# Kernel optimization log

Hardware: AMD Instinct MI355X
Metric: run time of the kernel (lower is better)

The kernel has to match this reference:

```python
import jax, jax.numpy as jnp
import numpy as np

N = 100000
E = 1600000
C = 128
NEG_SLOPE = 0.2
BN_EPS = 1e-5


def setup_inputs() -> dict:
    key = jax.random.key(0)
    ks = jax.random.split(key, 6)
    x = jax.random.normal(ks[0], (N, C), dtype=jnp.float32)
    edge_index = jax.random.randint(ks[1], (2, E), 0, N, dtype=jnp.int64)
    # Glorot-ish scaled params, stacked over the 3 layers (all 128->128)
    Ws = jax.random.normal(ks[2], (3, C, C), dtype=jnp.float32) * (1.0 / np.sqrt(C))
    att_srcs = jax.random.normal(ks[3], (3, C), dtype=jnp.float32) * (1.0 / np.sqrt(C))
    att_dsts = jax.random.normal(ks[4], (3, C), dtype=jnp.float32) * (1.0 / np.sqrt(C))
    biases = jnp.zeros((3, C), dtype=jnp.float32)
    gammas = jnp.ones((3, C), dtype=jnp.float32)
    betas = jnp.zeros((3, C), dtype=jnp.float32)
    return {"x": x, "edge_index": edge_index, "Ws": Ws, "att_srcs": att_srcs,
            "att_dsts": att_dsts, "biases": biases, "gammas": gammas, "betas": betas}


def _gat_layer(x, W, a_src, a_dst, bias, src, dst):
    # linear transform: [N, C]
    h = x @ W
    # per-node attention logits
    s_src = h @ a_src  # [N]
    s_dst = h @ a_dst  # [N]
    # edge-wise gather + leaky relu scoring
    e = jax.nn.leaky_relu(s_src[src] + s_dst[dst], NEG_SLOPE)  # [E+N]
    # scatter-softmax over incoming edges of each target node
    m = jax.ops.segment_max(e, dst, num_segments=N)  # every node has a self-loop
    ex = jnp.exp(e - m[dst])
    denom = jax.ops.segment_sum(ex, dst, num_segments=N)
    alpha = ex / denom[dst]  # [E+N]
    # scatter-add aggregation of alpha-weighted source features
    out = jax.ops.segment_sum(alpha[:, None] * h[src], dst, num_segments=N)
    return out + bias


def _batch_norm(x, gamma, beta):
    mu = jnp.mean(x, axis=0)
    var = jnp.mean(jnp.square(x - mu), axis=0)
    return gamma * (x - mu) * jax.lax.rsqrt(var + BN_EPS) + beta


def reference(x, edge_index, Ws, att_srcs, att_dsts, biases, gammas, betas):
    # PyG GATConv adds self-loops by default
    loops = jnp.arange(N, dtype=edge_index.dtype)
    src = jnp.concatenate([edge_index[0], loops])
    dst = jnp.concatenate([edge_index[1], loops])
    outs = []
    for l in range(3):
        x = _gat_layer(x, Ws[l], att_srcs[l], att_dsts[l], biases[l], src, dst)
        x = jax.nn.relu(x)
        x = _batch_norm(x, gammas[l], betas[l])
        outs.append(x)
    # jump=True: concat all layer outputs -> [N, 3*C]
    return jnp.concatenate(outs, axis=-1)
```

## Files before the change

kernel.cpp:

```cpp
#include <hip/hip_runtime.h>
#include <math.h>

#define N_NODES 100000
#define N_EDGES 1600000
#define M_TOT   (N_EDGES + N_NODES)
#define C_DIM   128
#define NEG_SLOPE 0.2f
#define BN_EPS 1e-5f

#define NBUCK 8
#define BUCK_NODES 12500
#define BUCK_CAP 240000

#define BN_NB 256
#define SCAN_NB 98

typedef _Float16 f16x8 __attribute__((ext_vector_type(8)));
typedef float f32x4 __attribute__((ext_vector_type(4)));

static __device__ __forceinline__ unsigned short f2h(float f) {
    _Float16 h = (_Float16)f;
    unsigned short u;
    __builtin_memcpy(&u, &h, 2);
    return u;
}
static __device__ __forceinline__ float h2f(unsigned short u) {
    _Float16 h;
    __builtin_memcpy(&h, &u, 2);
    return (float)h;
}
static __device__ __forceinline__ _Float16 f2h16(float f) { return (_Float16)f; }

__global__ void zero_i32(int* __restrict__ p, int n) {
    int i = blockIdx.x * blockDim.x + threadIdx.x;
    if (i < n) p[i] = 0;
}

__global__ __launch_bounds__(256) void conv_w(const float* __restrict__ Wall,
                                              unsigned short* __restrict__ Wh) {
    int i = blockIdx.x * 256 + threadIdx.x;
    if (i >= 3 * 128 * 128) return;
    int l = i >> 14;
    int r = i & 16383;
    int k = r >> 7;
    int n = r & 127;
    Wh[(size_t)l * 16384 + n * 128 + k] = f2h(Wall[i]);
}

__global__ __launch_bounds__(256) void bucket_edges(const int* __restrict__ ei,
                                                    int* __restrict__ bucket_next,
                                                    int2* __restrict__ buckets) {
    __shared__ int cnt[NBUCK];
    __shared__ int base[NBUCK];
    int tid = threadIdx.x;
    if (tid < NBUCK) cnt[tid] = 0;
    __syncthreads();
    int m = blockIdx.x * 256 + tid;
    int src = 0, dst = 0, p = 0, myoff = 0;
    bool valid = (m < M_TOT);
    if (valid) {
        if (m < N_EDGES) { src = ei[m]; dst = ei[N_EDGES + m]; }
        else             { src = m - N_EDGES; dst = src; }
        p = dst / BUCK_NODES;
        myoff = atomicAdd(&cnt[p], 1);
    }
    __syncthreads();
    if (tid < NBUCK) base[tid] = (cnt[tid] > 0) ? atomicAdd(&bucket_next[tid], cnt[tid]) : 0;
    __syncthreads();
    if (valid) {
        buckets[(size_t)p * BUCK_CAP + base[p] + myoff] = make_int2(src, dst);
    }
}

__global__ __launch_bounds__(256) void count_deg_b(const int2* __restrict__ buckets,
                                                   const int* __restrict__ bucket_next,
                                                   int* __restrict__ deg) {
    int p = blockIdx.x & 7;
    int chunk = blockIdx.x >> 3;
    int len = bucket_next[p];
    const int2* b = buckets + (size_t)p * BUCK_CAP;
    int stride = (gridDim.x >> 3) * 256;
    for (int i = chunk * 256 + threadIdx.x; i < len; i += stride) {
        atomicAdd(&deg[b[i].y], 1);
    }
}

__global__ __launch_bounds__(256) void scatter_b(const int2* __restrict__ buckets,
                                                 const int* __restrict__ bucket_next,
                                                 int* __restrict__ nextp,
                                                 int* __restrict__ csr_src) {
    int p = blockIdx.x & 7;
    int chunk = blockIdx.x >> 3;
    int len = bucket_next[p];
    const int2* b = buckets + (size_t)p * BUCK_CAP;
    int stride = (gridDim.x >> 3) * 256;
    for (int i = chunk * 256 + threadIdx.x; i < len; i += stride) {
        int2 e = b[i];
        int pos = atomicAdd(&nextp[e.y], 1);
        csr_src[pos] = e.x;
    }
}

__global__ __launch_bounds__(256) void block_sums(const int* __restrict__ deg,
                                                  int* __restrict__ partials) {
    __shared__ int lds[256];
    int base = blockIdx.x * 1024;
    int s = 0;
    for (int i = threadIdx.x; i < 1024; i += 256) {
        int idx = base + i;
        if (idx < N_NODES) s += deg[idx];
    }
    lds[threadIdx.x] = s;
    __syncthreads();
    for (int off = 128; off > 0; off >>= 1) {
        if (threadIdx.x < off) lds[threadIdx.x] += lds[threadIdx.x + off];
        __syncthreads();
    }
    if (threadIdx.x == 0) partials[blockIdx.x] = lds[0];
}

__global__ __launch_bounds__(128) void scan_partials(int* __restrict__ partials, int nb,
                                                     int* __restrict__ row_ptr) {
    __shared__ int lds[128];
    int tid = threadIdx.x;
    int v = (tid < nb) ? partials[tid] : 0;
    lds[tid] = v;
    __syncthreads();
    for (int off = 1; off < 128; off <<= 1) {
        int t = (tid >= off) ? lds[tid - off] : 0;
        __syncthreads();
        lds[tid] += t;
        __syncthreads();
    }
    if (tid < nb) partials[tid] = lds[tid] - v;
    if (tid == 0) row_ptr[N_NODES] = M_TOT;
}

__global__ __launch_bounds__(256) void scan_write(const int* __restrict__ deg,
                                                  const int* __restrict__ partials,
                                                  int* __restrict__ row_ptr,
                                                  int* __restrict__ nextp) {
    __shared__ int lds[256];
    int tid = threadIdx.x;
    int base = blockIdx.x * 1024;
    int i0 = base + tid * 4;
    int d[4];
#pragma unroll
    for (int t = 0; t < 4; ++t)
        d[t] = (i0 + t < N_NODES) ? deg[i0 + t] : 0;
    int tsum = d[0] + d[1] + d[2] + d[3];
    lds[tid] = tsum;
    __syncthreads();
    for (int off = 1; off < 256; off <<= 1) {
        int v = (tid >= off) ? lds[tid - off] : 0;
        __syncthreads();
        lds[tid] += v;
        __syncthreads();
    }
    int excl = lds[tid] - tsum;
    int run = partials[blockIdx.x] + excl;
#pragma unroll
    for (int t = 0; t < 4; ++t) {
        if (i0 + t < N_NODES) {
            row_ptr[i0 + t] = run;
            nextp[i0 + t]   = run;
            run += d[t];
        }
    }
}

__global__ __launch_bounds__(256, 2) void gemm_attn(
    const float* __restrict__ X, int ldx,
    const unsigned short* __restrict__ Wh,
    const float* __restrict__ a_src, const float* __restrict__ a_dst,
    const float* __restrict__ gbv,
    float* __restrict__ outw,
    unsigned short* __restrict__ Hh, float* __restrict__ Ssrc,
    float* __restrict__ Sdst) {
    int tid = threadIdx.x;
    int wave = tid >> 6;
    int lane = tid & 63;
    int q = lane >> 4;
    int l15 = lane & 15;
    int wrow = wave * 32;
    int rbase = blockIdx.x * 128;

    int row0 = rbase + wrow + l15;
    int row1 = row0 + 16;
    bool ok0 = row0 < N_NODES, ok1 = row1 < N_NODES;
    int r0c = ok0 ? row0 : (N_NODES - 1);
    int r1c = ok1 ? row1 : (N_NODES - 1);

    f32x4 acc[2][8] = {};

#pragma unroll
    for (int ks = 0; ks < 128; ks += 32) {
        int k0 = ks + q * 8;
        float4 v0 = *(const float4*)&X[(size_t)r0c * ldx + k0];
        float4 v1 = *(const float4*)&X[(size_t)r0c * ldx + k0 + 4];
        float4 u0 = *(const float4*)&X[(size_t)r1c * ldx + k0];
        float4 u1 = *(const float4*)&X[(size_t)r1c * ldx + k0 + 4];
        if (gbv) {
            float4 g0 = *(const float4*)&gbv[k0];
            float4 g1 = *(const float4*)&gbv[k0 + 4];
            float4 b0 = *(const float4*)&gbv[128 + k0];
            float4 b1 = *(const float4*)&gbv[128 + k0 + 4];
            v0.x = fmaf(v0.x, g0.x, b0.x); v0.y = fmaf(v0.y, g0.y, b0.y);
            v0.z = fmaf(v0.z, g0.z, b0.z); v0.w = fmaf(v0.w, g0.w, b0.w);
            v1.x = fmaf(v1.x, g1.x, b1.x); v1.y = fmaf(v1.y, g1.y, b1.y);
            v1.z = fmaf(v1.z, g1.z, b1.z); v1.w = fmaf(v1.w, g1.w, b1.w);
            u0.x = fmaf(u0.x, g0.x, b0.x); u0.y = fmaf(u0.y, g0.y, b0.y);
            u0.z = fmaf(u0.z, g0.z, b0.z); u0.w = fmaf(u0.w, g0.w, b0.w);
            u1.x = fmaf(u1.x, g1.x, b1.x); u1.y = fmaf(u1.y, g1.y, b1.y);
            u1.z = fmaf(u1.z, g1.z, b1.z); u1.w = fmaf(u1.w, g1.w, b1.w);
            if (ok0) {
                *(float4*)&outw[(size_t)row0 * 384 + k0] = v0;
                *(float4*)&outw[(size_t)row0 * 384 + k0 + 4] = v1;
            }
            if (ok1) {
                *(float4*)&outw[(size_t)row1 * 384 + k0] = u0;
                *(float4*)&outw[(size_t)row1 * 384 + k0 + 4] = u1;
            }
        }
        f16x8 a0, a1;
        a0[0] = f2h16(v0.x); a0[1] = f2h16(v0.y); a0[2] = f2h16(v0.z); a0[3] = f2h16(v0.w);
        a0[4] = f2h16(v1.x); a0[5] = f2h16(v1.y); a0[6] = f2h16(v1.z); a0[7] = f2h16(v1.w);
        a1[0] = f2h16(u0.x); a1[1] = f2h16(u0.y); a1[2] = f2h16(u0.z); a1[3] = f2h16(u0.w);
        a1[4] = f2h16(u1.x); a1[5] = f2h16(u1.y); a1[6] = f2h16(u1.z); a1[7] = f2h16(u1.w);
#pragma unroll
        for (int c = 0; c < 8; ++c) {
            f16x8 b = *(const f16x8*)&Wh[(size_t)(c * 16 + l15) * 128 + k0];
            acc[0][c] = __builtin_amdgcn_mfma_f32_16x16x32_f16(a0, b, acc[0][c], 0, 0, 0);
            acc[1][c] = __builtin_amdgcn_mfma_f32_16x16x32_f16(a1, b, acc[1][c], 0, 0, 0);
        }
    }

    float avs[8], avd[8];
#pragma unroll
    for (int c = 0; c < 8; ++c) {
        avs[c] = a_src[c * 16 + l15];
        avd[c] = a_dst[c * 16 + l15];
    }
#pragma unroll
    for (int r = 0; r < 2; ++r) {
        float ps[4] = {0, 0, 0, 0}, pd[4] = {0, 0, 0, 0};
#pragma unroll
        for (int g = 0; g < 4; ++g) {
            int row = rbase + wrow + r * 16 + q * 4 + g;
            bool ok = (row < N_NODES);
#pragma unroll
            for (int c = 0; c < 8; ++c) {
                float h = acc[r][c][g];
                if (ok) Hh[(size_t)row * 128 + c * 16 + l15] = f2h(h);
                ps[g] = fmaf(h, avs[c], ps[g]);
                pd[g] = fmaf(h, avd[c], pd[g]);
            }
        }
#pragma unroll
        for (int g = 0; g < 4; ++g) {
#pragma unroll
            for (int off = 1; off < 16; off <<= 1) {
                ps[g] += __shfl_xor(ps[g], off, 64);
                pd[g] += __shfl_xor(pd[g], off, 64);
            }
        }
        if (l15 == 0) {
#pragma unroll
            for (int g = 0; g < 4; ++g) {
                int row = rbase + wrow + r * 16 + q * 4 + g;
                if (row < N_NODES) {
                    Ssrc[row] = ps[g];
                    Sdst[row] = pd[g];
                }
            }
        }
    }
}

__global__ __launch_bounds__(256) void aggregate(
    const unsigned short* __restrict__ Hh, const int* __restrict__ row_ptr,
    const int* __restrict__ csr_src,
    const float* __restrict__ Ssrc, const float* __restrict__ Sdst,
    const float* __restrict__ bias, float* __restrict__ Y) {
    int wave = threadIdx.x >> 6;
    int lane = threadIdx.x & 63;
    int g = lane >> 4;
    int l15 = lane & 15;
    int v = blockIdx.x * 4 + wave;
    int start = row_ptr[v];
    int end = row_ptr[v + 1];
    float sdv = Sdst[v];

    float sself = Ssrc[v] + sdv;
    float m = (sself > 0.0f) ? sself : NEG_SLOPE * sself;

    float acc[8] = {0, 0, 0, 0, 0, 0, 0, 0};
    float denom = 0.0f;

    int j = start;
    for (; j + 16 <= end; j += 16) {
        int u0 = csr_src[j + g];
        int u1 = csr_src[j + 4 + g];
        int u2 = csr_src[j + 8 + g];
        int u3 = csr_src[j + 12 + g];
        float ss0 = Ssrc[u0];
        float ss1 = Ssrc[u1];
        float ss2 = Ssrc[u2];
        float ss3 = Ssrc[u3];
        f16x8 h0 = *(const f16x8*)&Hh[(size_t)u0 * 128 + l15 * 8];
        f16x8 h1 = *(const f16x8*)&Hh[(size_t)u1 * 128 + l15 * 8];
        f16x8 h2 = *(const f16x8*)&Hh[(size_t)u2 * 128 + l15 * 8];
        f16x8 h3 = *(const f16x8*)&Hh[(size_t)u3 * 128 + l15 * 8];
        float s0 = ss0 + sdv; s0 = (s0 > 0.0f) ? s0 : NEG_SLOPE * s0;
        float s1 = ss1 + sdv; s1 = (s1 > 0.0f) ? s1 : NEG_SLOPE * s1;
        float s2 = ss2 + sdv; s2 = (s2 > 0.0f) ? s2 : NEG_SLOPE * s2;
        float s3 = ss3 + sdv; s3 = (s3 > 0.0f) ? s3 : NEG_SLOPE * s3;
        float w0 = __expf(s0 - m);
        float w1 = __expf(s1 - m);
        float w2 = __expf(s2 - m);
        float w3 = __expf(s3 - m);
        denom += (w0 + w1) + (w2 + w3);
#pragma unroll
        for (int i = 0; i < 8; ++i) acc[i] = fmaf(w0, (float)h0[i], acc[i]);
#pragma unroll
        for (int i = 0; i < 8; ++i) acc[i] = fmaf(w1, (float)h1[i], acc[i]);
#pragma unroll
        for (int i = 0; i < 8; ++i) acc[i] = fmaf(w2, (float)h2[i], acc[i]);
#pragma unroll
        for (int i = 0; i < 8; ++i) acc[i] = fmaf(w3, (float)h3[i], acc[i]);
    }
    for (; j + 8 <= end; j += 8) {
        int u0 = csr_src[j + g];
        int u1 = csr_src[j + 4 + g];
        float ss0 = Ssrc[u0];
        float ss1 = Ssrc[u1];
        f16x8 h0 = *(const f16x8*)&Hh[(size_t)u0 * 128 + l15 * 8];
        f16x8 h1 = *(const f16x8*)&Hh[(size_t)u1 * 128 + l15 * 8];
        float s0 = ss0 + sdv; s0 = (s0 > 0.0f) ? s0 : NEG_SLOPE * s0;
        float s1 = ss1 + sdv; s1 = (s1 > 0.0f) ? s1 : NEG_SLOPE * s1;
        float w0 = __expf(s0 - m);
        float w1 = __expf(s1 - m);
        denom += w0 + w1;
#pragma unroll
        for (int i = 0; i < 8; ++i) acc[i] = fmaf(w0, (float)h0[i], acc[i]);
#pragma unroll
        for (int i = 0; i < 8; ++i) acc[i] = fmaf(w1, (float)h1[i], acc[i]);
    }
    for (; j < end; j += 4) {
        int je = j + g;
        bool ok = (je < end);
        int u = ok ? csr_src[je] : v;
        float s = Ssrc[u] + sdv; s = (s > 0.0f) ? s : NEG_SLOPE * s;
        float w = ok ? __expf(s - m) : 0.0f;
        f16x8 h = *(const f16x8*)&Hh[(size_t)u * 128 + l15 * 8];
        denom += w;
#pragma unroll
        for (int i = 0; i < 8; ++i) acc[i] = fmaf(w, (float)h[i], acc[i]);
    }

#pragma unroll
    for (int i = 0; i < 8; ++i) {
        acc[i] += __shfl_xor(acc[i], 16, 64);
        acc[i] += __shfl_xor(acc[i], 32, 64);
    }
    denom += __shfl_xor(denom, 16, 64);
    denom += __shfl_xor(denom, 32, 64);

    if (g == 0) {
        float inv = 1.0f / denom;
        float4 b0 = *(const float4*)&bias[l15 * 8];
        float4 b1 = *(const float4*)&bias[l15 * 8 + 4];
        float4 o0, o1;
        o0.x = fmaxf(fmaf(acc[0], inv, b0.x), 0.0f);
        o0.y = fmaxf(fmaf(acc[1], inv, b0.y), 0.0f);
        o0.z = fmaxf(fmaf(acc[2], inv, b0.z), 0.0f);
        o0.w = fmaxf(fmaf(acc[3], inv, b0.w), 0.0f);
        o1.x = fmaxf(fmaf(acc[4], inv, b1.x), 0.0f);
        o1.y = fmaxf(fmaf(acc[5], inv, b1.y), 0.0f);
        o1.z = fmaxf(fmaf(acc[6], inv, b1.z), 0.0f);
        o1.w = fmaxf(fmaf(acc[7], inv, b1.w), 0.0f);
        *(float4*)&Y[(size_t)v * 128 + l15 * 8] = o0;
        *(float4*)&Y[(size_t)v * 128 + l15 * 8 + 4] = o1;
    }
}

__global__ __launch_bounds__(256) void bn_stats(const float* __restrict__ Y,
                                                float* __restrict__ partial) {
    __shared__ float red[256 * 8];
    int tid = threadIdx.x;
    int rowlane = tid >> 5;
    int cg = tid & 31;
    float4 s = make_float4(0, 0, 0, 0);
    float4 qq = make_float4(0, 0, 0, 0);
    for (int i = blockIdx.x * 8 + rowlane; i < N_NODES; i += BN_NB * 8) {
        float4 v = *(const float4*)&Y[(size_t)i * 128 + cg * 4];
        s.x += v.x; s.y += v.y; s.z += v.z; s.w += v.w;
        qq.x = fmaf(v.x, v.x, qq.x);
        qq.y = fmaf(v.y, v.y, qq.y);
        qq.z = fmaf(v.z, v.z, qq.z);
        qq.w = fmaf(v.w, v.w, qq.w);
    }
    float* r = &red[tid * 8];
    r[0] = s.x; r[1] = s.y; r[2] = s.z; r[3] = s.w;
    r[4] = qq.x; r[5] = qq.y; r[6] = qq.z; r[7] = qq.w;
    __syncthreads();
    for (int off = 4; off > 0; off >>= 1) {
        if (rowlane < off) {
            float* o = &red[(tid + off * 32) * 8];
#pragma unroll
            for (int t = 0; t < 8; ++t) r[t] += o[t];
        }
        __syncthreads();
    }
    if (rowlane == 0) {
        *(float4*)&partial[(size_t)blockIdx.x * 256 + cg * 4] =
            make_float4(r[0], r[1], r[2], r[3]);
        *(float4*)&partial[(size_t)blockIdx.x * 256 + 128 + cg * 4] =
            make_float4(r[4], r[5], r[6], r[7]);
    }
}

__global__ __launch_bounds__(256) void bn_finalize(const float* __restrict__ partial,
                                                   const float* __restrict__ gamma,
                                                   const float* __restrict__ beta,
                                                   float* __restrict__ gb) {
    __shared__ float tot[256];
    int tid = threadIdx.x;
    float acc = 0.0f;
    for (int b = 0; b < BN_NB; ++b) acc += partial[(size_t)b * 256 + tid];
    tot[tid] = acc;
    __syncthreads();
    if (tid < 128) {
        const float invN = 1.0f / (float)N_NODES;
        float mu = tot[tid] * invN;
        float var = tot[128 + tid] * invN - mu * mu;
        float g = gamma[tid] * rsqrtf(var + BN_EPS);
        gb[tid] = g;
        gb[128 + tid] = beta[tid] - mu * g;
    }
}

__global__ __launch_bounds__(256) void bn_apply(const float* __restrict__ Y,
                                                const float* __restrict__ gb,
                                                float* __restrict__ out) {
    int idx = blockIdx.x * blockDim.x + threadIdx.x;
    if (idx >= N_NODES * 32) return;
    int row = idx >> 5;
    int c4 = (idx & 31) * 4;
    float4 v = *(const float4*)&Y[(size_t)row * 128 + c4];
    float4 g = *(const float4*)&gb[c4];
    float4 b = *(const float4*)&gb[128 + c4];
    v.x = fmaf(v.x, g.x, b.x);
    v.y = fmaf(v.y, g.y, b.y);
    v.z = fmaf(v.z, g.z, b.z);
    v.w = fmaf(v.w, g.w, b.w);
    *(float4*)&out[(size_t)row * 384 + c4] = v;
}

extern "C" void kernel_launch(void* const* d_in, const int* in_sizes, int n_in,
                              void* d_out, int out_size, void* d_ws, size_t ws_size,
                              hipStream_t stream) {
    const float* x      = (const float*)d_in[0];
    const int*   ei     = (const int*)d_in[1];
    const float* Wall   = (const float*)d_in[2];
    const float* asrcs  = (const float*)d_in[3];
    const float* adsts  = (const float*)d_in[4];
    const float* biases = (const float*)d_in[5];
    const float* gammas = (const float*)d_in[6];
    const float* betas  = (const float*)d_in[7];
    float* out = (float*)d_out;

    unsigned short* Hh = (unsigned short*)d_ws;
    float* Y       = (float*)(Hh + (size_t)N_NODES * 128);
    float* Ssrc    = Y + (size_t)N_NODES * 128;
    float* Sdst    = Ssrc + N_NODES;
    float* bnpart  = Sdst + N_NODES;
    float* gb      = bnpart + BN_NB * 256;
    unsigned short* Wh = (unsigned short*)(gb + 256);
    int* deg       = (int*)(Wh + 3 * 128 * 128);
    int* bucket_next = deg + N_NODES;
    int* row_ptr   = bucket_next + NBUCK;
    int* nextp     = row_ptr + (N_NODES + 1);
    int* partials  = nextp + N_NODES;
    int* csr_src   = partials + 128;
    int2* buckets  = (int2*)(csr_src + M_TOT + 2);

    const int ZERO_CNT = N_NODES + NBUCK;
    const int NB_EDGE = (M_TOT + 255) / 256;
    const int NB_PART = 2048;

    zero_i32<<<(ZERO_CNT + 255) / 256, 256, 0, stream>>>(deg, ZERO_CNT);
    conv_w<<<192, 256, 0, stream>>>(Wall, Wh);
    bucket_edges<<<NB_EDGE, 256, 0, stream>>>(ei, bucket_next, buckets);
    count_deg_b<<<NB_PART, 256, 0, stream>>>(buckets, bucket_next, deg);
    block_sums<<<SCAN_NB, 256, 0, stream>>>(deg, partials);
    scan_partials<<<1, 128, 0, stream>>>(partials, SCAN_NB, row_ptr);
    scan_write<<<SCAN_NB, 256, 0, stream>>>(deg, partials, row_ptr, nextp);
    scatter_b<<<NB_PART, 256, 0, stream>>>(buckets, bucket_next, nextp, csr_src);

    for (int l = 0; l < 3; ++l) {
        const float* xin;
        int ldx;
        const float* gbl;
        float* outw;
        if (l == 0) { xin = x; ldx = 128; gbl = nullptr; outw = nullptr; }
        else        { xin = Y; ldx = 128; gbl = gb; outw = out + (size_t)(l - 1) * 128; }
        gemm_attn<<<(N_NODES + 127) / 128, 256, 0, stream>>>(
            xin, ldx, Wh + (size_t)l * 128 * 128,
            asrcs + l * 128, adsts + l * 128, gbl, outw, Hh, Ssrc, Sdst);
        aggregate<<<N_NODES / 4, 256, 0, stream>>>(
            Hh, row_ptr, csr_src, Ssrc, Sdst, biases + l * 128, Y);
        bn_stats<<<BN_NB, 256, 0, stream>>>(Y, bnpart);
        bn_finalize<<<1, 256, 0, stream>>>(bnpart, gammas + l * 128,
                                           betas + l * 128, gb);
    }
    bn_apply<<<(N_NODES * 32 + 255) / 256, 256, 0, stream>>>(
        Y, gb, out + (size_t)2 * 128);
}
```

Before: 792.8 us.

## Fuse degree count into bucketing and stage GEMM output through LDS

Degree counting now happens in the bucket_edges kernel via global atomics, which removes the separate count_deg_b pass over the bucketed edges. gemm_attn is retiled to 64 rows per block with one 16-row MFMA tile per wave and higher occupancy bounds. Its fp16 H output is staged through padded shared memory so it can be written with coalesced 16-byte stores instead of scattered 2-byte stores. The trade-off is random global atomics on deg during bucketing, plus a block barrier and some LDS traffic in the GEMM.

```diff
diff --git a/kernel.cpp b/kernel.cpp
--- a/kernel.cpp
+++ b/kernel.cpp
@@ -14,6 +14,7 @@
 
 #define BN_NB 256
 #define SCAN_NB 98
+#define HS_LD 136
 
 typedef _Float16 f16x8 __attribute__((ext_vector_type(8)));
 typedef float f32x4 __attribute__((ext_vector_type(4)));
@@ -49,7 +50,8 @@
 
 __global__ __launch_bounds__(256) void bucket_edges(const int* __restrict__ ei,
                                                     int* __restrict__ bucket_next,
-                                                    int2* __restrict__ buckets) {
+                                                    int2* __restrict__ buckets,
+                                                    int* __restrict__ deg) {
     __shared__ int cnt[NBUCK];
     __shared__ int base[NBUCK];
     int tid = threadIdx.x;
@@ -63,25 +65,13 @@
         else             { src = m - N_EDGES; dst = src; }
         p = dst / BUCK_NODES;
         myoff = atomicAdd(&cnt[p], 1);
+        atomicAdd(&deg[dst], 1);
     }
     __syncthreads();
     if (tid < NBUCK) base[tid] = (cnt[tid] > 0) ? atomicAdd(&bucket_next[tid], cnt[tid]) : 0;
     __syncthreads();
     if (valid) {
         buckets[(size_t)p * BUCK_CAP + base[p] + myoff] = make_int2(src, dst);
-    }
-}
-
-__global__ __launch_bounds__(256) void count_deg_b(const int2* __restrict__ buckets,
-                                                   const int* __restrict__ bucket_next,
-                                                   int* __restrict__ deg) {
-    int p = blockIdx.x & 7;
-    int chunk = blockIdx.x >> 3;
-    int len = bucket_next[p];
-    const int2* b = buckets + (size_t)p * BUCK_CAP;
-    int stride = (gridDim.x >> 3) * 256;
-    for (int i = chunk * 256 + threadIdx.x; i < len; i += stride) {
-        atomicAdd(&deg[b[i].y], 1);
     }
 }
 
@@ -169,7 +159,7 @@
     }
 }
 
-__global__ __launch_bounds__(256, 2) void gemm_attn(
+__global__ __launch_bounds__(256, 4) void gemm_attn(
     const float* __restrict__ X, int ldx,
     const unsigned short* __restrict__ Wh,
     const float* __restrict__ a_src, const float* __restrict__ a_dst,
@@ -177,29 +167,26 @@
     float* __restrict__ outw,
     unsigned short* __restrict__ Hh, float* __restrict__ Ssrc,
     float* __restrict__ Sdst) {
+    __shared__ unsigned short Hs[64 * HS_LD];
     int tid = threadIdx.x;
     int wave = tid >> 6;
     int lane = tid & 63;
     int q = lane >> 4;
     int l15 = lane & 15;
-    int wrow = wave * 32;
-    int rbase = blockIdx.x * 128;
+    int wrow = wave * 16;
+    int rbase = blockIdx.x * 64;
 
     int row0 = rbase + wrow + l15;
-    int row1 = row0 + 16;
-    bool ok0 = row0 < N_NODES, ok1 = row1 < N_NODES;
+    bool ok0 = row0 < N_NODES;
     int r0c = ok0 ? row0 : (N_NODES - 1);
-    int r1c = ok1 ? row1 : (N_NODES - 1);
-
-    f32x4 acc[2][8] = {};
+
+    f32x4 acc[8] = {};
 
 #pragma unroll
     for (int ks = 0; ks < 128; ks += 32) {
         int k0 = ks + q * 8;
         float4 v0 = *(const float4*)&X[(size_t)r0c * ldx + k0];
         float4 v1 = *(const float4*)&X[(size_t)r0c * ldx + k0 + 4];
-        float4 u0 = *(const float4*)&X[(size_t)r1c * ldx + k0];
-        float4 u1 = *(const float4*)&X[(size_t)r1c * ldx + k0 + 4];
         if (gbv) {
             float4 g0 = *(const float4*)&gbv[k0];
             float4 g1 = *(const float4*)&gbv[k0 + 4];
@@ -209,29 +196,18 @@
             v0.z = fmaf(v0.z, g0.z, b0.z); v0.w = fmaf(v0.w, g0.w, b0.w);
             v1.x = fmaf(v1.x, g1.x, b1.x); v1.y = fmaf(v1.y, g1.y, b1.y);
             v1.z = fmaf(v1.z, g1.z, b1.z); v1.w = fmaf(v1.w, g1.w, b1.w);
-            u0.x = fmaf(u0.x, g0.x, b0.x); u0.y = fmaf(u0.y, g0.y, b0.y);
-            u0.z = fmaf(u0.z, g0.z, b0.z); u0.w = fmaf(u0.w, g0.w, b0.w);
-            u1.x = fmaf(u1.x, g1.x, b1.x); u1.y = fmaf(u1.y, g1.y, b1.y);
-            u1.z = fmaf(u1.z, g1.z, b1.z); u1.w = fmaf(u1.w, g1.w, b1.w);
             if (ok0) {
                 *(float4*)&outw[(size_t)row0 * 384 + k0] = v0;
                 *(float4*)&outw[(size_t)row0 * 384 + k0 + 4] = v1;
             }
-            if (ok1) {
-                *(float4*)&outw[(size_t)row1 * 384 + k0] = u0;
-                *(float4*)&outw[(size_t)row1 * 384 + k0 + 4] = u1;
-            }
-        }
-        f16x8 a0, a1;
-        a0[0] = f2h16(v0.x); a0[1] = f2h16(v0.y); a0[2] = f2h16(v0.z); a0[3] = f2h16(v0.w);
-        a0[4] = f2h16(v1.x); a0[5] = f2h16(v1.y); a0[6] = f2h16(v1.z); a0[7] = f2h16(v1.w);
-        a1[0] = f2h16(u0.x); a1[1] = f2h16(u0.y); a1[2] = f2h16(u0.z); a1[3] = f2h16(u0.w);
-        a1[4] = f2h16(u1.x); a1[5] = f2h16(u1.y); a1[6] = f2h16(u1.z); a1[7] = f2h16(u1.w);
+        }
+        f16x8 a;
+        a[0] = f2h16(v0.x); a[1] = f2h16(v0.y); a[2] = f2h16(v0.z); a[3] = f2h16(v0.w);
+        a[4] = f2h16(v1.x); a[5] = f2h16(v1.y); a[6] = f2h16(v1.z); a[7] = f2h16(v1.w);
 #pragma unroll
         for (int c = 0; c < 8; ++c) {
             f16x8 b = *(const f16x8*)&Wh[(size_t)(c * 16 + l15) * 128 + k0];
-            acc[0][c] = __builtin_amdgcn_mfma_f32_16x16x32_f16(a0, b, acc[0][c], 0, 0, 0);
-            acc[1][c] = __builtin_amdgcn_mfma_f32_16x16x32_f16(a1, b, acc[1][c], 0, 0, 0);
+            acc[c] = __builtin_amdgcn_mfma_f32_16x16x32_f16(a, b, acc[c], 0, 0, 0);
         }
     }
 
@@ -241,38 +217,52 @@
         avs[c] = a_src[c * 16 + l15];
         avd[c] = a_dst[c * 16 + l15];
     }
-#pragma unroll
-    for (int r = 0; r < 2; ++r) {
-        float ps[4] = {0, 0, 0, 0}, pd[4] = {0, 0, 0, 0};
+    float ps[4] = {0, 0, 0, 0}, pd[4] = {0, 0, 0, 0};
+#pragma unroll
+    for (int g = 0; g < 4; ++g) {
+#pragma unroll
+        for (int c = 0; c < 8; ++c) {
+            float h = acc[c][g];
+            ps[g] = fmaf(h, avs[c], ps[g]);
+            pd[g] = fmaf(h, avd[c], pd[g]);
+        }
+    }
+#pragma unroll
+    for (int g = 0; g < 4; ++g) {
+#pragma unroll
+        for (int off = 1; off < 16; off <<= 1) {
+            ps[g] += __shfl_xor(ps[g], off, 64);
+            pd[g] += __shfl_xor(pd[g], off, 64);
+        }
+    }
+    if (l15 == 0) {
 #pragma unroll
         for (int g = 0; g < 4; ++g) {
-            int row = rbase + wrow + r * 16 + q * 4 + g;
-            bool ok = (row < N_NODES);
-#pragma unroll
-            for (int c = 0; c < 8; ++c) {
-                float h = acc[r][c][g];
-                if (ok) Hh[(size_t)row * 128 + c * 16 + l15] = f2h(h);
-                ps[g] = fmaf(h, avs[c], ps[g]);
-                pd[g] = fmaf(h, avd[c], pd[g]);
+            int row = rbase + wrow + q * 4 + g;
+            if (row < N_NODES) {
+                Ssrc[row] = ps[g];
+                Sdst[row] = pd[g];
             }
         }
+    }
+
+#pragma unroll
+    for (int c = 0; c < 8; ++c) {
 #pragma unroll
         for (int g = 0; g < 4; ++g) {
-#pragma unroll
-            for (int off = 1; off < 16; off <<= 1) {
-                ps[g] += __shfl_xor(ps[g], off, 64);
-                pd[g] += __shfl_xor(pd[g], off, 64);
-            }
-        }
-        if (l15 == 0) {
-#pragma unroll
-            for (int g = 0; g < 4; ++g) {
-                int row = rbase + wrow + r * 16 + q * 4 + g;
-                if (row < N_NODES) {
-                    Ssrc[row] = ps[g];
-                    Sdst[row] = pd[g];
-                }
-            }
+            Hs[(wrow + q * 4 + g) * HS_LD + c * 16 + l15] = f2h(acc[c][g]);
+        }
+    }
+    __syncthreads();
+#pragma unroll
+    for (int i = 0; i < 4; ++i) {
+        int idx = i * 256 + tid;
+        int lr = idx >> 4;
+        int cg = (idx & 15) * 8;
+        int grow = rbase + lr;
+        if (grow < N_NODES) {
+            *(f16x8*)&Hh[(size_t)grow * 128 + cg] =
+                *(const f16x8*)&Hs[lr * HS_LD + cg];
         }
     }
 }
@@ -491,8 +481,7 @@
 
     zero_i32<<<(ZERO_CNT + 255) / 256, 256, 0, stream>>>(deg, ZERO_CNT);
     conv_w<<<192, 256, 0, stream>>>(Wall, Wh);
-    bucket_edges<<<NB_EDGE, 256, 0, stream>>>(ei, bucket_next, buckets);
-    count_deg_b<<<NB_PART, 256, 0, stream>>>(buckets, bucket_next, deg);
+    bucket_edges<<<NB_EDGE, 256, 0, stream>>>(ei, bucket_next, buckets, deg);
     block_sums<<<SCAN_NB, 256, 0, stream>>>(deg, partials);
     scan_partials<<<1, 128, 0, stream>>>(partials, SCAN_NB, row_ptr);
     scan_write<<<SCAN_NB, 256, 0, stream>>>(deg, partials, row_ptr, nextp);
@@ -505,7 +494,7 @@
         float* outw;
         if (l == 0) { xin = x; ldx = 128; gbl = nullptr; outw = nullptr; }
         else        { xin = Y; ldx = 128; gbl = gb; outw = out + (size_t)(l - 1) * 128; }
-        gemm_attn<<<(N_NODES + 127) / 128, 256, 0, stream>>>(
+        gemm_attn<<<(N_NODES + 63) / 64, 256, 0, stream>>>(
             xin, ldx, Wh + (size_t)l * 128 * 128,
             asrcs + l * 128, adsts + l * 128, gbl, outw, Hh, Ssrc, Sdst);
         aggregate<<<N_NODES / 4, 256, 0, stream>>>(
```

Result: faster. 767.1 us (-3.2%).
